# Optimization experiments

Measured on AMD Instinct MI355X. Metric: run time of the kernel, lower is better.

The kernel has to match this reference:

```python
import jax, jax.numpy as jnp
import numpy as np

BANDWIDTH = 0.5  # init kwarg


def setup_inputs() -> dict:
    key = jax.random.key(0)
    k1, k2 = jax.random.split(key)
    samples = jax.random.normal(k1, (2, 4096, 6), dtype=jnp.float32)    # [B, N, D]
    locations = jax.random.normal(k2, (2048, 6), dtype=jnp.float32)    # [L, D]
    return {"samples": samples, "locations": locations}


def reference(samples, locations):
    # Pairwise squared distances: ||samples - locations||^2 over D
    # torch: norm(...)**2 == sum of squares (same math, cleaner gradient)
    d = samples[None, :, :, :] - locations[:, None, None, :]   # [L, B, N, D]
    diff2 = jnp.sum(d * d, axis=-1)                            # [L, B, N]
    out = jnp.exp(-diff2 / (2.0 * BANDWIDTH ** 2)).sum(axis=-1)  # [L, B]
    norm = out.sum(axis=0)                                     # [B]
    # torch broadcasting of [L,B] / [1,1,B] yields [1,L,B]
    pdf = out / norm.reshape(1, 1, -1)                          # [1, L, B]
    return pdf
```

## Files before the change

kernel.cpp:

```cpp
#include <hip/hip_runtime.h>


#define KDE_B 2
#define KDE_N 4096
#define KDE_D 6

#define NEG2_LOG2E (-2.8853900817779268f)

__global__ void kde_main_kernel(const float* __restrict__ samples,
                                const float* __restrict__ locations,
                                float* __restrict__ out, int L) {
    const int w    = (blockIdx.x * blockDim.x + threadIdx.x) >> 6;
    const int lane = threadIdx.x & 63;
    const int l = w >> 1;
    const int b = w & 1;
    if (l >= L) return;

    float loc[KDE_D];
#pragma unroll
    for (int d = 0; d < KDE_D; ++d) loc[d] = locations[l * KDE_D + d];

    const float* sp = samples + (size_t)b * KDE_N * KDE_D;

    float acc = 0.f;
    for (int n = lane; n < KDE_N; n += 64) {
        const float* s = sp + n * KDE_D;
        float2 s01 = *reinterpret_cast<const float2*>(s);
        float2 s23 = *reinterpret_cast<const float2*>(s + 2);
        float2 s45 = *reinterpret_cast<const float2*>(s + 4);
        float d0 = s01.x - loc[0];
        float d1 = s01.y - loc[1];
        float d2 = s23.x - loc[2];
        float d3 = s23.y - loc[3];
        float d4 = s45.x - loc[4];
        float d5 = s45.y - loc[5];
        float diff2 = d0 * d0;
        diff2 = fmaf(d1, d1, diff2);
        diff2 = fmaf(d2, d2, diff2);
        diff2 = fmaf(d3, d3, diff2);
        diff2 = fmaf(d4, d4, diff2);
        diff2 = fmaf(d5, d5, diff2);
        acc += exp2f(diff2 * NEG2_LOG2E);
    }

#pragma unroll
    for (int off = 32; off >= 1; off >>= 1)
        acc += __shfl_xor(acc, off, 64);

    if (lane == 0) out[l * KDE_B + b] = acc;
}

__global__ void kde_normalize_kernel(float* __restrict__ out, int L) {
    const int b   = blockIdx.x;
    const int tid = threadIdx.x;

    float s = 0.f;
    for (int l = tid; l < L; l += 256) s += out[l * KDE_B + b];

#pragma unroll
    for (int off = 32; off >= 1; off >>= 1)
        s += __shfl_xor(s, off, 64);

    __shared__ float red[4];
    if ((tid & 63) == 0) red[tid >> 6] = s;
    __syncthreads();
    const float inv = 1.f / (red[0] + red[1] + red[2] + red[3]);

    for (int l = tid; l < L; l += 256) out[l * KDE_B + b] *= inv;
}

extern "C" void kernel_launch(void* const* d_in, const int* in_sizes, int n_in,
                              void* d_out, int out_size, void* d_ws, size_t ws_size,
                              hipStream_t stream) {
    const float* samples   = (const float*)d_in[0];
    const float* locations = (const float*)d_in[1];
    float* out = (float*)d_out;

    const int L = in_sizes[1] / KDE_D;
    const int waves = L * KDE_B;
    const int threads = 256;
    const int blocks = (waves * 64 + threads - 1) / threads;

    kde_main_kernel<<<blocks, threads, 0, stream>>>(samples, locations, out, L);
    kde_normalize_kernel<<<KDE_B, 256, 0, stream>>>(out, L);
}
```

Measured before the change: 78.99 us.

## Tile KDE over location and sample chunks with LDS staging and expanded distance

Restructures the main kernel into 2D tiles: each block stages a 256-sample chunk in LDS with a precomputed scaled squared norm, and each thread handles 4 locations, so every sample load is reused across several locations. The squared distance is expanded into norms plus a dot product, which folds the scaling into FMA coefficients, and the raw hardware exp2 builtin is used. Partial sums per chunk go to a workspace and a finalize kernel reduces them and normalizes. Sizes are now hardcoded to L=2048, and the expanded form can lose some precision when sample and location are close.

```diff
diff --git a/kernel.cpp b/kernel.cpp
--- a/kernel.cpp
+++ b/kernel.cpp
@@ -4,69 +4,133 @@
 #define KDE_B 2
 #define KDE_N 4096
 #define KDE_D 6
+#define KDE_L 2048
 
 #define NEG2_LOG2E (-2.8853900817779268f)
 
-__global__ void kde_main_kernel(const float* __restrict__ samples,
-                                const float* __restrict__ locations,
-                                float* __restrict__ out, int L) {
-    const int w    = (blockIdx.x * blockDim.x + threadIdx.x) >> 6;
-    const int lane = threadIdx.x & 63;
-    const int l = w >> 1;
-    const int b = w & 1;
-    if (l >= L) return;
+#define TL 128
+#define LPT 4
+#define NC 256
+#define NCHUNK (KDE_N / NC)
+#define LTILES (KDE_L / TL)
 
-    float loc[KDE_D];
+__global__ void __launch_bounds__(256, 2)
+kde_main_kernel(const float* __restrict__ samples,
+                const float* __restrict__ locations,
+                float* __restrict__ ws) {
+    const int bid = blockIdx.x;
+    const int b  = bid & 1;
+    const int c  = (bid >> 1) & (NCHUNK - 1);
+    const int lt = bid >> 5;
+
+    const int tid = threadIdx.x;
+    const int g   = tid >> 3;
+    const int sub = tid & 7;
+
+    __shared__ float lds[NC * 8];
+
+    {
+        const float* sp = samples + ((size_t)b * KDE_N + (size_t)c * NC + tid) * KDE_D;
+        float2 s01 = *reinterpret_cast<const float2*>(sp);
+        float2 s23 = *reinterpret_cast<const float2*>(sp + 2);
+        float2 s45 = *reinterpret_cast<const float2*>(sp + 4);
+        float s2 = s01.x * s01.x;
+        s2 = fmaf(s01.y, s01.y, s2);
+        s2 = fmaf(s23.x, s23.x, s2);
+        s2 = fmaf(s23.y, s23.y, s2);
+        s2 = fmaf(s45.x, s45.x, s2);
+        s2 = fmaf(s45.y, s45.y, s2);
+        float4* dst = reinterpret_cast<float4*>(&lds[tid * 8]);
+        dst[0] = make_float4(s01.x, s01.y, s23.x, s23.y);
+        dst[1] = make_float4(s45.x, s45.y, NEG2_LOG2E * s2, 0.f);
+    }
+
+    const int lbase = lt * TL + g * LPT;
+    float lp[LPT][KDE_D];
+    float A[LPT];
 #pragma unroll
-    for (int d = 0; d < KDE_D; ++d) loc[d] = locations[l * KDE_D + d];
+    for (int j = 0; j < LPT; ++j) {
+        const float* q = locations + (size_t)(lbase + j) * KDE_D;
+        float l2 = 0.f;
+#pragma unroll
+        for (int d = 0; d < KDE_D; ++d) {
+            float v = q[d];
+            l2 = fmaf(v, v, l2);
+            lp[j][d] = (-2.0f * NEG2_LOG2E) * v;
+        }
+        A[j] = NEG2_LOG2E * l2;
+    }
 
-    const float* sp = samples + (size_t)b * KDE_N * KDE_D;
+    float acc[LPT] = {0.f, 0.f, 0.f, 0.f};
 
-    float acc = 0.f;
-    for (int n = lane; n < KDE_N; n += 64) {
-        const float* s = sp + n * KDE_D;
-        float2 s01 = *reinterpret_cast<const float2*>(s);
-        float2 s23 = *reinterpret_cast<const float2*>(s + 2);
-        float2 s45 = *reinterpret_cast<const float2*>(s + 4);
-        float d0 = s01.x - loc[0];
-        float d1 = s01.y - loc[1];
-        float d2 = s23.x - loc[2];
-        float d3 = s23.y - loc[3];
-        float d4 = s45.x - loc[4];
-        float d5 = s45.y - loc[5];
-        float diff2 = d0 * d0;
-        diff2 = fmaf(d1, d1, diff2);
-        diff2 = fmaf(d2, d2, diff2);
-        diff2 = fmaf(d3, d3, diff2);
-        diff2 = fmaf(d4, d4, diff2);
-        diff2 = fmaf(d5, d5, diff2);
-        acc += exp2f(diff2 * NEG2_LOG2E);
+    __syncthreads();
+
+    const float4* lds4 = reinterpret_cast<const float4*>(lds);
+#pragma unroll 4
+    for (int k = 0; k < NC / 8; ++k) {
+        const int n = (k << 3) | sub;
+        float4 sA = lds4[n * 2];
+        float4 sB = lds4[n * 2 + 1];
+#pragma unroll
+        for (int j = 0; j < LPT; ++j) {
+            float e = fmaf(sA.x, lp[j][0], A[j]);
+            e = fmaf(sA.y, lp[j][1], e);
+            e = fmaf(sA.z, lp[j][2], e);
+            e = fmaf(sA.w, lp[j][3], e);
+            e = fmaf(sB.x, lp[j][4], e);
+            e = fmaf(sB.y, lp[j][5], e);
+            e += sB.z;
+            acc[j] += __builtin_amdgcn_exp2f(e);
+        }
+    }
+
+#pragma unroll
+    for (int j = 0; j < LPT; ++j) {
+        float v = acc[j];
+        v += __shfl_xor(v, 1, 64);
+        v += __shfl_xor(v, 2, 64);
+        v += __shfl_xor(v, 4, 64);
+        acc[j] = v;
+    }
+    if (sub == 0) {
+#pragma unroll
+        for (int j = 0; j < LPT; ++j)
+            ws[((size_t)b * NCHUNK + c) * KDE_L + lbase + j] = acc[j];
+    }
+}
+
+__global__ void kde_finalize_kernel(const float* __restrict__ ws,
+                                    float* __restrict__ out) {
+    const int b   = blockIdx.x;
+    const int tid = threadIdx.x;
+    const float* base = ws + (size_t)b * NCHUNK * KDE_L;
+
+    float vals[KDE_L / 256];
+    float norm = 0.f;
+#pragma unroll
+    for (int i = 0; i < KDE_L / 256; ++i) {
+        const int l = tid + i * 256;
+        float s = 0.f;
+#pragma unroll
+        for (int c = 0; c < NCHUNK; ++c)
+            s += base[c * KDE_L + l];
+        vals[i] = s;
+        norm += s;
     }
 
 #pragma unroll
     for (int off = 32; off >= 1; off >>= 1)
-        acc += __shfl_xor(acc, off, 64);
-
-    if (lane == 0) out[l * KDE_B + b] = acc;
-}
-
-__global__ void kde_normalize_kernel(float* __restrict__ out, int L) {
-    const int b   = blockIdx.x;
-    const int tid = threadIdx.x;
-
-    float s = 0.f;
-    for (int l = tid; l < L; l += 256) s += out[l * KDE_B + b];
-
-#pragma unroll
-    for (int off = 32; off >= 1; off >>= 1)
-        s += __shfl_xor(s, off, 64);
-
+        norm += __shfl_xor(norm, off, 64);
     __shared__ float red[4];
-    if ((tid & 63) == 0) red[tid >> 6] = s;
+    if ((tid & 63) == 0) red[tid >> 6] = norm;
     __syncthreads();
     const float inv = 1.f / (red[0] + red[1] + red[2] + red[3]);
 
-    for (int l = tid; l < L; l += 256) out[l * KDE_B + b] *= inv;
+#pragma unroll
+    for (int i = 0; i < KDE_L / 256; ++i) {
+        const int l = tid + i * 256;
+        out[l * KDE_B + b] = vals[i] * inv;
+    }
 }
 
 extern "C" void kernel_launch(void* const* d_in, const int* in_sizes, int n_in,
@@ -75,12 +139,9 @@
     const float* samples   = (const float*)d_in[0];
     const float* locations = (const float*)d_in[1];
     float* out = (float*)d_out;
+    float* ws  = (float*)d_ws;
 
-    const int L = in_sizes[1] / KDE_D;
-    const int waves = L * KDE_B;
-    const int threads = 256;
-    const int blocks = (waves * 64 + threads - 1) / threads;
-
-    kde_main_kernel<<<blocks, threads, 0, stream>>>(samples, locations, out, L);
-    kde_normalize_kernel<<<KDE_B, 256, 0, stream>>>(out, L);
+    const int blocks = LTILES * NCHUNK * KDE_B;
+    kde_main_kernel<<<blocks, 256, 0, stream>>>(samples, locations, ws);
+    kde_finalize_kernel<<<KDE_B, 256, 0, stream>>>(ws, out);
 }
```

Measured after the change: 63.50 us. 1.24x faster.
